# Optimization experiments

Measured on AMD Instinct MI355X. Metric: run time of the kernel, lower is better.

Reference implementation:

```python
import jax, jax.numpy as jnp
import numpy as np

N_NODES = 100000
N_EDGES = 1600000
D_FEAT = 32


def setup_inputs() -> dict:
    key = jax.random.key(0)
    k1, k2, k3, k4, k5 = jax.random.split(key, 5)
    src_feats = jax.random.normal(k1, (N_NODES, D_FEAT), dtype=jnp.float32)
    cj = jax.random.uniform(k2, (N_NODES, 1), dtype=jnp.float32)
    ci = jax.random.uniform(k3, (N_NODES, 1), dtype=jnp.float32)
    src_idx = jax.random.randint(k4, (N_EDGES,), 0, N_NODES, dtype=jnp.int32)
    dst_idx = jax.random.randint(k5, (N_EDGES,), 0, N_NODES, dtype=jnp.int32)
    return {"src_feats": src_feats, "cj": cj, "ci": ci,
            "src_idx": src_idx, "dst_idx": dst_idx}


def reference(src_feats, cj, ci, src_idx, dst_idx):
    # Dropout in eval mode (identity). Training-mode dropout is stochastic and
    # excluded from the correctness baseline.
    weighted = src_feats * cj                      # [N, d] scale by src norm coeff
    msgs = weighted[src_idx]                       # [E, d] gather (copy_u)
    agg = jax.ops.segment_sum(msgs, dst_idx, num_segments=N_NODES)  # [N, d] sum aggregate
    return agg * ci                                # [N, d] scale by dst norm coeff
```

## Files before the change

### kernel.cpp

```cpp
#include <hip/hip_runtime.h>

#define N_NODES 100000
#define N_EDGES 1600000
#define D_FEAT 32
#define CAP 48
#define NPASS 16
#define NODES_PER_PASS ((N_NODES + NPASS - 1) / NPASS)
#define THREADS_PER_PASS (N_EDGES / 4)
#define BLOCKS_PER_PASS ((THREADS_PER_PASS + 255) / 256)

__global__ __launch_bounds__(256) void lgc_bucket(
    const int4*  __restrict__ dst4,
    const int4*  __restrict__ src4,
    const float* __restrict__ src_feats,
    const float* __restrict__ cj,
    int*         __restrict__ cnt,
    int*         __restrict__ bucket,
    float*       __restrict__ out)
{
    int pass = blockIdx.x / BLOCKS_PER_PASS;
    int lb   = blockIdx.x % BLOCKS_PER_PASS;
    int t = lb * 256 + threadIdx.x;
    if (t >= THREADS_PER_PASS) return;

    const int lo = pass * NODES_PER_PASS;
    const int hi = lo + NODES_PER_PASS;

    int4 d4 = dst4[t];
    bool ix = (d4.x >= lo) & (d4.x < hi);
    bool iy = (d4.y >= lo) & (d4.y < hi);
    bool iz = (d4.z >= lo) & (d4.z < hi);
    bool iw = (d4.w >= lo) & (d4.w < hi);
    if (!(ix | iy | iz | iw)) return;

    int4 s4 = src4[t];
    int ds[4] = {d4.x, d4.y, d4.z, d4.w};
    int ss[4] = {s4.x, s4.y, s4.z, s4.w};
    bool in[4] = {ix, iy, iz, iw};

    #pragma unroll
    for (int k = 0; k < 4; ++k) {
        if (!in[k]) continue;
        int d = ds[k], s = ss[k];
        int pos = atomicAdd(&cnt[d], 1);
        if (pos < CAP) {
            bucket[(size_t)d * CAP + pos] = s;
        } else {
            float c = cj[s];
            const float* row = src_feats + (size_t)s * D_FEAT;
            float* o = out + (size_t)d * D_FEAT;
            for (int f = 0; f < D_FEAT; ++f) atomicAdd(o + f, row[f] * c);
        }
    }
}

__global__ __launch_bounds__(256) void lgc_gather(
    const float4* __restrict__ feats4,
    const float*  __restrict__ cj,
    const float*  __restrict__ ci,
    const int*    __restrict__ cnt,
    const int*    __restrict__ bucket,
    float4*       __restrict__ out4)
{
    int tid = blockIdx.x * 256 + threadIdx.x;
    int n = tid >> 3;
    int f = tid & 7;

    int c = cnt[n];
    if (c > CAP) c = CAP;
    const int4* b4 = (const int4*)(bucket + (size_t)n * CAP);

    float4 acc = make_float4(0.f, 0.f, 0.f, 0.f);
    for (int i = 0; i < c; i += 4) {
        int4 bv = b4[i >> 2];
        int m = c - i;
        {
            float w = cj[bv.x];
            float4 v = feats4[(size_t)bv.x * 8 + f];
            acc.x += v.x * w; acc.y += v.y * w; acc.z += v.z * w; acc.w += v.w * w;
        }
        if (m > 1) {
            float w = cj[bv.y];
            float4 v = feats4[(size_t)bv.y * 8 + f];
            acc.x += v.x * w; acc.y += v.y * w; acc.z += v.z * w; acc.w += v.w * w;
        }
        if (m > 2) {
            float w = cj[bv.z];
            float4 v = feats4[(size_t)bv.z * 8 + f];
            acc.x += v.x * w; acc.y += v.y * w; acc.z += v.z * w; acc.w += v.w * w;
        }
        if (m > 3) {
            float w = cj[bv.w];
            float4 v = feats4[(size_t)bv.w * 8 + f];
            acc.x += v.x * w; acc.y += v.y * w; acc.z += v.z * w; acc.w += v.w * w;
        }
    }

    float s = ci[n];
    float4 o = out4[tid];
    acc.x = (acc.x + o.x) * s;
    acc.y = (acc.y + o.y) * s;
    acc.z = (acc.z + o.z) * s;
    acc.w = (acc.w + o.w) * s;
    out4[tid] = acc;
}

__global__ __launch_bounds__(256) void lgc_scatter(
    const float4* __restrict__ src_feats4,
    const float*  __restrict__ cj,
    const int*    __restrict__ src_idx,
    const int*    __restrict__ dst_idx,
    float*        __restrict__ out)
{
    long tid = (long)blockIdx.x * blockDim.x + threadIdx.x;
    const long total = (long)N_EDGES * 8;
    if (tid >= total) return;
    int e  = (int)(tid >> 3);
    int f4 = (int)(tid & 7);
    int s = src_idx[e];
    int d = dst_idx[e];
    float c = cj[s];
    float4 v = src_feats4[s * 8 + f4];
    float* o = out + (size_t)d * D_FEAT + f4 * 4;
    atomicAdd(o + 0, v.x * c);
    atomicAdd(o + 1, v.y * c);
    atomicAdd(o + 2, v.z * c);
    atomicAdd(o + 3, v.w * c);
}

__global__ __launch_bounds__(256) void lgc_scale(
    float4*       __restrict__ out4,
    const float*  __restrict__ ci)
{
    int tid = blockIdx.x * blockDim.x + threadIdx.x;
    const int total = N_NODES * 8;
    if (tid >= total) return;
    float c = ci[tid >> 3];
    float4 v = out4[tid];
    v.x *= c; v.y *= c; v.z *= c; v.w *= c;
    out4[tid] = v;
}

extern "C" void kernel_launch(void* const* d_in, const int* in_sizes, int n_in,
                              void* d_out, int out_size, void* d_ws, size_t ws_size,
                              hipStream_t stream) {
    const float* src_feats = (const float*)d_in[0];
    const float* cj        = (const float*)d_in[1];
    const float* ci        = (const float*)d_in[2];
    const int*   src_idx   = (const int*)d_in[3];
    const int*   dst_idx   = (const int*)d_in[4];
    float*       out       = (float*)d_out;

    const size_t cnt_ints    = 102400;
    const size_t bucket_ints = (size_t)N_NODES * CAP;
    const size_t need = (cnt_ints + bucket_ints) * sizeof(int);

    if (ws_size >= need) {
        int* cnt    = (int*)d_ws;
        int* bucket = cnt + cnt_ints;

        hipMemsetAsync(cnt, 0, N_NODES * sizeof(int), stream);
        hipMemsetAsync(out, 0, (size_t)out_size * sizeof(float), stream);

        lgc_bucket<<<NPASS * BLOCKS_PER_PASS, 256, 0, stream>>>(
            (const int4*)dst_idx, (const int4*)src_idx, src_feats, cj,
            cnt, bucket, out);

        lgc_gather<<<(N_NODES * 8) / 256, 256, 0, stream>>>(
            (const float4*)src_feats, cj, ci, cnt, bucket, (float4*)out);
    } else {
        hipMemsetAsync(out, 0, (size_t)out_size * sizeof(float), stream);
        {
            const long total = (long)N_EDGES * 8;
            const int grid = (int)((total + 255) / 256);
            lgc_scatter<<<grid, 256, 0, stream>>>((const float4*)src_feats, cj,
                                                  src_idx, dst_idx, out);
        }
        {
            const int grid = (N_NODES * 8 + 255) / 256;
            lgc_scale<<<grid, 256, 0, stream>>>((float4*)out, ci);
        }
    }
}
```

Before: 206.1 us.

## Partition bucket pass by XCD via interleaved blocks, shrink bucket cap, preload indices

The bucket kernel now interleaves blocks across 8 destination-node ranges using blockIdx modulo 8. With round-robin block dispatch, each XCD's L2 then sees atomics for only its own slice of counters and buckets. This replaces 16 sequential passes over the edge list with 8 interleaved ones, so the index arrays are read fewer times. The bucket capacity drops from 48 to 32, shrinking the bucket array, and the gather kernel preloads all bucket index vectors into registers with a fully unrolled loop to expose more memory parallelism. In exchange, more edges overflow the cap (average degree is 16) and fall back to slow per-feature atomic adds, and the unrolled gather uses more registers.

```diff
diff --git a/kernel.cpp b/kernel.cpp
--- a/kernel.cpp
+++ b/kernel.cpp
@@ -3,11 +3,11 @@
 #define N_NODES 100000
 #define N_EDGES 1600000
 #define D_FEAT 32
-#define CAP 48
-#define NPASS 16
-#define NODES_PER_PASS ((N_NODES + NPASS - 1) / NPASS)
-#define THREADS_PER_PASS (N_EDGES / 4)
-#define BLOCKS_PER_PASS ((THREADS_PER_PASS + 255) / 256)
+#define CAP 32
+#define NXCD 8
+#define NODES_PER_XCD (N_NODES / NXCD)
+#define EDGE_THREADS (N_EDGES / 4)
+#define EDGE_BLOCKS ((EDGE_THREADS + 255) / 256)
 
 __global__ __launch_bounds__(256) void lgc_bucket(
     const int4*  __restrict__ dst4,
@@ -18,13 +18,13 @@
     int*         __restrict__ bucket,
     float*       __restrict__ out)
 {
-    int pass = blockIdx.x / BLOCKS_PER_PASS;
-    int lb   = blockIdx.x % BLOCKS_PER_PASS;
-    int t = lb * 256 + threadIdx.x;
-    if (t >= THREADS_PER_PASS) return;
+    int x  = blockIdx.x % NXCD;
+    int lb = blockIdx.x / NXCD;
+    int t  = lb * 256 + threadIdx.x;
+    if (t >= EDGE_THREADS) return;
 
-    const int lo = pass * NODES_PER_PASS;
-    const int hi = lo + NODES_PER_PASS;
+    const int lo = x * NODES_PER_XCD;
+    const int hi = lo + NODES_PER_XCD;
 
     int4 d4 = dst4[t];
     bool ix = (d4.x >= lo) & (d4.x < hi);
@@ -70,29 +70,37 @@
     if (c > CAP) c = CAP;
     const int4* b4 = (const int4*)(bucket + (size_t)n * CAP);
 
+    int4 r[8];
+    #pragma unroll
+    for (int j = 0; j < 8; ++j)
+        if (j * 4 < c) r[j] = b4[j];
+
     float4 acc = make_float4(0.f, 0.f, 0.f, 0.f);
-    for (int i = 0; i < c; i += 4) {
-        int4 bv = b4[i >> 2];
-        int m = c - i;
-        {
-            float w = cj[bv.x];
-            float4 v = feats4[(size_t)bv.x * 8 + f];
-            acc.x += v.x * w; acc.y += v.y * w; acc.z += v.z * w; acc.w += v.w * w;
-        }
-        if (m > 1) {
-            float w = cj[bv.y];
-            float4 v = feats4[(size_t)bv.y * 8 + f];
-            acc.x += v.x * w; acc.y += v.y * w; acc.z += v.z * w; acc.w += v.w * w;
-        }
-        if (m > 2) {
-            float w = cj[bv.z];
-            float4 v = feats4[(size_t)bv.z * 8 + f];
-            acc.x += v.x * w; acc.y += v.y * w; acc.z += v.z * w; acc.w += v.w * w;
-        }
-        if (m > 3) {
-            float w = cj[bv.w];
-            float4 v = feats4[(size_t)bv.w * 8 + f];
-            acc.x += v.x * w; acc.y += v.y * w; acc.z += v.z * w; acc.w += v.w * w;
+    #pragma unroll
+    for (int j = 0; j < 8; ++j) {
+        int base = j * 4;
+        if (base < c) {
+            int4 bv = r[j];
+            {
+                float w = cj[bv.x];
+                float4 v = feats4[(size_t)bv.x * 8 + f];
+                acc.x += v.x * w; acc.y += v.y * w; acc.z += v.z * w; acc.w += v.w * w;
+            }
+            if (base + 1 < c) {
+                float w = cj[bv.y];
+                float4 v = feats4[(size_t)bv.y * 8 + f];
+                acc.x += v.x * w; acc.y += v.y * w; acc.z += v.z * w; acc.w += v.w * w;
+            }
+            if (base + 2 < c) {
+                float w = cj[bv.z];
+                float4 v = feats4[(size_t)bv.z * 8 + f];
+                acc.x += v.x * w; acc.y += v.y * w; acc.z += v.z * w; acc.w += v.w * w;
+            }
+            if (base + 3 < c) {
+                float w = cj[bv.w];
+                float4 v = feats4[(size_t)bv.w * 8 + f];
+                acc.x += v.x * w; acc.y += v.y * w; acc.z += v.z * w; acc.w += v.w * w;
+            }
         }
     }
 
@@ -162,7 +170,7 @@
         hipMemsetAsync(cnt, 0, N_NODES * sizeof(int), stream);
         hipMemsetAsync(out, 0, (size_t)out_size * sizeof(float), stream);
 
-        lgc_bucket<<<NPASS * BLOCKS_PER_PASS, 256, 0, stream>>>(
+        lgc_bucket<<<NXCD * EDGE_BLOCKS, 256, 0, stream>>>(
             (const int4*)dst_idx, (const int4*)src_idx, src_feats, cj,
             cnt, bucket, out);
 
```

New measurement: 181.6 us. 11.9% less time.
